# Performance work log

Hardware: AMD Instinct MI355X
Metric: run time of the kernel (lower is better)

The kernel has to match this reference:

```python
import jax, jax.numpy as jnp
import numpy as np

B, C, N, K_CAND, K_TOP = 8, 16, 65536, 10, 4

def setup_inputs() -> dict:
    key = jax.random.key(0)
    k1, k2, k3, k4, k5, k6 = jax.random.split(key, 6)
    scale = 1.0 / np.sqrt(2 * C)  # conv2d default init scale for fan_in=32
    return {
        "original_features": jax.random.normal(k1, (B, C, N), dtype=jnp.float32),
        "sampled_features": jax.random.normal(k2, (B, C, N, K_CAND), dtype=jnp.float32),
        "w1": jax.random.uniform(k3, (2 * C,), jnp.float32, -scale, scale),
        "b1": jax.random.uniform(k4, (), jnp.float32, -scale, scale),
        "w2": jax.random.uniform(k5, (2 * C,), jnp.float32, -scale, scale),
        "b2": jax.random.uniform(k6, (), jnp.float32, -scale, scale),
    }

def reference(original_features, sampled_features, w1, b1, w2, b2):
    # original_features: [B,C,N]; sampled_features: [B,C,N,K_CAND]
    # 1x1 conv over concat([repeated_orig, sampled]) == two channel contractions
    wo1, ws1 = w1[:C], w1[C:]
    # similarity scores: [B,N,K_CAND]
    sim = jax.nn.sigmoid(
        jnp.einsum('bcn,c->bn', original_features, wo1)[:, :, None]
        + jnp.einsum('bcnk,c->bnk', sampled_features, ws1)
        + b1)
    _, topk_idx = jax.lax.top_k(sim, K_TOP)  # [B,N,K_TOP]
    idx = jnp.broadcast_to(topk_idx[:, None, :, :], (sim.shape[0], C, sim.shape[1], K_TOP))
    topk_features = jnp.take_along_axis(sampled_features, idx, axis=-1)  # [B,C,N,K_TOP]
    wo2, ws2 = w2[:C], w2[C:]
    recal = jax.nn.sigmoid(
        jnp.einsum('bcn,c->bn', original_features, wo2)[:, :, None]
        + jnp.einsum('bcnk,c->bnk', topk_features, ws2)
        + b2)  # [B,N,K_TOP]
    summed = jnp.einsum('bcnk,bnk->bcn', topk_features, recal)
    return original_features + summed
```

## Files before the change

kernel.cpp:

```cpp
#include <hip/hip_runtime.h>
#include <math.h>

#define BB 8
#define CC 16
#define NN 65536
#define KC 10
#define KT 4

__global__ __launch_bounds__(256) void swg_kernel(
    const float* __restrict__ orig,
    const float* __restrict__ samp,
    const float* __restrict__ w1,
    const float* __restrict__ w2,
    const float* __restrict__ b2p,
    float* __restrict__ out)
{
    const int t = blockIdx.x * blockDim.x + threadIdx.x;
    const int q = t & 3;
    const int p = t >> 2;
    const int n = p & (NN - 1);
    const int b = p >> 16;

    const float b2 = b2p[0];

    float ws1[4], wo2[4], ws2[4];
#pragma unroll
    for (int cc = 0; cc < 4; ++cc) {
        const int c = q * 4 + cc;
        ws1[cc] = w1[CC + c];
        wo2[cc] = w2[c];
        ws2[cc] = w2[CC + c];
    }

    float v[4][KC];
    float o[4];
#pragma unroll
    for (int cc = 0; cc < 4; ++cc) {
        const int c = q * 4 + cc;
        const size_t base = (size_t)(b * CC + c) * NN + n;
        o[cc] = orig[base];
        const float2* sp = (const float2*)(samp + base * KC);
#pragma unroll
        for (int j = 0; j < 5; ++j) {
            const float2 x = sp[j];
            v[cc][2 * j]     = x.x;
            v[cc][2 * j + 1] = x.y;
        }
    }

    float s[KC], d2[KC];
    float dO = 0.f;
#pragma unroll
    for (int k = 0; k < KC; ++k) { s[k] = 0.f; d2[k] = 0.f; }
#pragma unroll
    for (int cc = 0; cc < 4; ++cc) {
        dO += o[cc] * wo2[cc];
#pragma unroll
        for (int k = 0; k < KC; ++k) {
            s[k]  += v[cc][k] * ws1[cc];
            d2[k] += v[cc][k] * ws2[cc];
        }
    }

#pragma unroll
    for (int m = 1; m <= 2; m <<= 1) {
        dO += __shfl_xor(dO, m, 64);
#pragma unroll
        for (int k = 0; k < KC; ++k) {
            s[k]  += __shfl_xor(s[k],  m, 64);
            d2[k] += __shfl_xor(d2[k], m, 64);
        }
    }

    unsigned selmask = 0;
#pragma unroll
    for (int t4 = 0; t4 < KT; ++t4) {
        float best = -INFINITY;
        int bi = 0;
#pragma unroll
        for (int k = 0; k < KC; ++k) {
            const bool avail  = ((selmask >> k) & 1u) == 0u;
            const bool better = avail && (s[k] > best);
            best = better ? s[k] : best;
            bi   = better ? k : bi;
        }
        selmask |= (1u << bi);
    }

    float w[KC];
#pragma unroll
    for (int k = 0; k < KC; ++k) {
        const float x = dO + d2[k] + b2;
        const float sig = 1.f / (1.f + __expf(-x));
        w[k] = ((selmask >> k) & 1u) ? sig : 0.f;
    }

#pragma unroll
    for (int cc = 0; cc < 4; ++cc) {
        float sum = 0.f;
#pragma unroll
        for (int k = 0; k < KC; ++k) sum += v[cc][k] * w[k];
        const int c = q * 4 + cc;
        const size_t base = (size_t)(b * CC + c) * NN + n;
        out[base] = o[cc] + sum;
    }
}

extern "C" void kernel_launch(void* const* d_in, const int* in_sizes, int n_in,
                              void* d_out, int out_size, void* d_ws, size_t ws_size,
                              hipStream_t stream) {
    const float* orig = (const float*)d_in[0];
    const float* samp = (const float*)d_in[1];
    const float* w1   = (const float*)d_in[2];
    const float* w2   = (const float*)d_in[4];
    const float* b2   = (const float*)d_in[5];
    float* out = (float*)d_out;

    const int total_threads = BB * NN * 4;
    const int block = 256;
    const int grid = total_threads / block;
    hipLaunchKernelGGL(swg_kernel, dim3(grid), dim3(block), 0, stream,
                       orig, samp, w1, w2, b2, out);
}
```

Baseline: 84.05 us.

## Stage sampled features through LDS via global_load_lds with 8 lanes per point

Sampled features are now loaded with coalesced 16-byte global_load_lds transfers into per-wave LDS tiles, replacing strided float2 loads straight from global memory. Each point is handled by 8 lanes with 2 channels each, reductions use three shuffle steps, top-k selection becomes a rank-counting pass, and the sigmoid uses a hardware reciprocal. The aim is better memory coalescing and more parallelism on a bandwidth-bound kernel, at the cost of more shuffles and LDS traffic per point.

```diff
diff --git a/kernel.cpp b/kernel.cpp
--- a/kernel.cpp
+++ b/kernel.cpp
@@ -7,7 +7,15 @@
 #define KC 10
 #define KT 4
 
-__global__ __launch_bounds__(256) void swg_kernel(
+#define PTW 8
+#define BLK 128
+#define PTB 16
+#define WFLT (PTW * CC * KC)
+
+typedef __attribute__((address_space(3))) void lds_t;
+typedef __attribute__((address_space(1))) void glob_t;
+
+__global__ __launch_bounds__(BLK, 8) void swg_kernel(
     const float* __restrict__ orig,
     const float* __restrict__ samp,
     const float* __restrict__ w1,
@@ -15,95 +23,111 @@
     const float* __restrict__ b2p,
     float* __restrict__ out)
 {
-    const int t = blockIdx.x * blockDim.x + threadIdx.x;
-    const int q = t & 3;
-    const int p = t >> 2;
-    const int n = p & (NN - 1);
-    const int b = p >> 16;
+    __shared__ float buf[2 * WFLT];
 
-    const float b2 = b2p[0];
+    const int t   = threadIdx.x;
+    const int l   = t & 63;
+    const int w   = t >> 6;
+    const int bid = blockIdx.x;
 
-    float ws1[4], wo2[4], ws2[4];
+    const int b   = bid >> 12;
+    const int n0w = ((bid * PTB) & (NN - 1)) + w * PTW;
+
+    const float4* sampB4 = (const float4*)samp
+        + (size_t)b * ((size_t)CC * NN * KC / 4);
+    const int n0q = n0w * (KC / 2) / 2;
+
+    float* ldsw = buf + w * WFLT;
+
 #pragma unroll
-    for (int cc = 0; cc < 4; ++cc) {
-        const int c = q * 4 + cc;
+    for (int j = 0; j < 5; ++j) {
+        const int m = j * 64 + l;
+        const int c = m / 20;
+        const int r = m - c * 20;
+        __builtin_amdgcn_global_load_lds(
+            (const glob_t*)(sampB4 + (size_t)c * (NN * KC / 4) + n0q + r),
+            (lds_t*)((char*)ldsw + j * 1024), 16, 0, 0);
+    }
+
+    const int q = l & 7;
+    const int p = l >> 3;
+    const int n = n0w + p;
+
+    float o[2];
+#pragma unroll
+    for (int cc = 0; cc < 2; ++cc)
+        o[cc] = orig[(size_t)(b * CC + q + 8 * cc) * NN + n];
+
+    float ws1[2], wo2[2], ws2[2];
+#pragma unroll
+    for (int cc = 0; cc < 2; ++cc) {
+        const int c = q + 8 * cc;
         ws1[cc] = w1[CC + c];
         wo2[cc] = w2[c];
         ws2[cc] = w2[CC + c];
     }
+    const float b2 = b2p[0];
 
-    float v[4][KC];
-    float o[4];
+    asm volatile("s_waitcnt vmcnt(0)" ::: "memory");
+
+    float v[2][KC];
 #pragma unroll
-    for (int cc = 0; cc < 4; ++cc) {
-        const int c = q * 4 + cc;
-        const size_t base = (size_t)(b * CC + c) * NN + n;
-        o[cc] = orig[base];
-        const float2* sp = (const float2*)(samp + base * KC);
+    for (int cc = 0; cc < 2; ++cc) {
+        const float* base = ldsw + (q + 8 * cc) * (PTW * KC) + p * KC;
 #pragma unroll
         for (int j = 0; j < 5; ++j) {
-            const float2 x = sp[j];
+            const float2 x = *(const float2*)(base + 2 * j);
             v[cc][2 * j]     = x.x;
             v[cc][2 * j + 1] = x.y;
         }
     }
 
-    float s[KC], d2[KC];
-    float dO = 0.f;
+    float s[KC];
+    float dO = o[0] * wo2[0] + o[1] * wo2[1];
 #pragma unroll
-    for (int k = 0; k < KC; ++k) { s[k] = 0.f; d2[k] = 0.f; }
+    for (int k = 0; k < KC; ++k)
+        s[k] = v[0][k] * ws1[0] + v[1][k] * ws1[1];
 #pragma unroll
-    for (int cc = 0; cc < 4; ++cc) {
-        dO += o[cc] * wo2[cc];
-#pragma unroll
-        for (int k = 0; k < KC; ++k) {
-            s[k]  += v[cc][k] * ws1[cc];
-            d2[k] += v[cc][k] * ws2[cc];
-        }
-    }
-
-#pragma unroll
-    for (int m = 1; m <= 2; m <<= 1) {
+    for (int m = 1; m <= 4; m <<= 1) {
         dO += __shfl_xor(dO, m, 64);
 #pragma unroll
-        for (int k = 0; k < KC; ++k) {
-            s[k]  += __shfl_xor(s[k],  m, 64);
-            d2[k] += __shfl_xor(d2[k], m, 64);
-        }
+        for (int k = 0; k < KC; ++k) s[k] += __shfl_xor(s[k], m, 64);
     }
 
     unsigned selmask = 0;
 #pragma unroll
-    for (int t4 = 0; t4 < KT; ++t4) {
-        float best = -INFINITY;
-        int bi = 0;
+    for (int k = 0; k < KC; ++k) {
+        int rk = 0;
 #pragma unroll
-        for (int k = 0; k < KC; ++k) {
-            const bool avail  = ((selmask >> k) & 1u) == 0u;
-            const bool better = avail && (s[k] > best);
-            best = better ? s[k] : best;
-            bi   = better ? k : bi;
+        for (int j = 0; j < KC; ++j) {
+            if (j == k) continue;
+            const bool beats = (j < k) ? (s[j] >= s[k]) : (s[j] > s[k]);
+            rk += beats ? 1 : 0;
         }
-        selmask |= (1u << bi);
+        selmask |= (rk < KT) ? (1u << k) : 0u;
     }
 
-    float w[KC];
+    float d2[KC];
+#pragma unroll
+    for (int k = 0; k < KC; ++k)
+        d2[k] = v[0][k] * ws2[0] + v[1][k] * ws2[1];
+#pragma unroll
+    for (int m = 1; m <= 4; m <<= 1) {
+#pragma unroll
+        for (int k = 0; k < KC; ++k) d2[k] += __shfl_xor(d2[k], m, 64);
+    }
+
+    float sum0 = 0.f, sum1 = 0.f;
 #pragma unroll
     for (int k = 0; k < KC; ++k) {
-        const float x = dO + d2[k] + b2;
-        const float sig = 1.f / (1.f + __expf(-x));
-        w[k] = ((selmask >> k) & 1u) ? sig : 0.f;
+        const float x   = dO + d2[k] + b2;
+        const float sig = __builtin_amdgcn_rcpf(1.f + __expf(-x));
+        const float wk  = ((selmask >> k) & 1u) ? sig : 0.f;
+        sum0 += v[0][k] * wk;
+        sum1 += v[1][k] * wk;
     }
-
-#pragma unroll
-    for (int cc = 0; cc < 4; ++cc) {
-        float sum = 0.f;
-#pragma unroll
-        for (int k = 0; k < KC; ++k) sum += v[cc][k] * w[k];
-        const int c = q * 4 + cc;
-        const size_t base = (size_t)(b * CC + c) * NN + n;
-        out[base] = o[cc] + sum;
-    }
+    out[(size_t)(b * CC + q)     * NN + n] = o[0] + sum0;
+    out[(size_t)(b * CC + q + 8) * NN + n] = o[1] + sum1;
 }
 
 extern "C" void kernel_launch(void* const* d_in, const int* in_sizes, int n_in,
@@ -116,9 +140,7 @@
     const float* b2   = (const float*)d_in[5];
     float* out = (float*)d_out;
 
-    const int total_threads = BB * NN * 4;
-    const int block = 256;
-    const int grid = total_threads / block;
-    hipLaunchKernelGGL(swg_kernel, dim3(grid), dim3(block), 0, stream,
+    const int grid = (BB * NN) / PTB;
+    hipLaunchKernelGGL(swg_kernel, dim3(grid), dim3(BLK), 0, stream,
                        orig, samp, w1, w2, b2, out);
 }
```

After: 88.33 us. +5.1%, slower.
